# Kernel optimization log

Measured on AMD Instinct MI355X. Metric: run time of the kernel, lower is better.

Reference implementation:

```python
import jax, jax.numpy as jnp
import numpy as np
from jax.scipy.special import logsumexp

NUM_TAGS = 64
BATCH = 512
SEQ = 1024


def setup_inputs() -> dict:
    key = jax.random.key(0)
    k1, k2, k3, k4, k5 = jax.random.split(key, 5)
    emissions = jax.random.normal(k1, (BATCH, SEQ, NUM_TAGS), dtype=jnp.float32)
    # parameters: uniform(-0.1, 0.1) as in reset_parameters
    start_transitions = jax.random.uniform(k2, (NUM_TAGS,), minval=-0.1, maxval=0.1, dtype=jnp.float32)
    end_transitions = jax.random.uniform(k3, (NUM_TAGS,), minval=-0.1, maxval=0.1, dtype=jnp.float32)
    transitions = jax.random.uniform(k4, (NUM_TAGS, NUM_TAGS), minval=-0.1, maxval=0.1, dtype=jnp.float32)
    tags = jax.random.randint(k5, (BATCH, SEQ), 0, NUM_TAGS, dtype=jnp.int64)
    mask = jnp.ones((BATCH, SEQ), dtype=bool)
    return {"emissions": emissions, "start_transitions": start_transitions,
            "end_transitions": end_transitions, "transitions": transitions,
            "tags": tags, "mask": mask}


def _crf_loss(emissions, start_transitions, end_transitions, transitions, tags, mask):
    # batch_first=True -> move to time-major (S, B, T)
    emissions = jnp.transpose(emissions, (1, 0, 2))
    tags = tags.T
    mask = mask.T
    S, B, T = emissions.shape
    maskf = mask.astype(emissions.dtype)

    # ---- joint (numerator) score, fully vectorized ----
    em_sc = jnp.take_along_axis(emissions, tags[:, :, None], axis=2)[:, :, 0]  # [S, B]
    trans_sc = transitions[tags[:-1], tags[1:]]                                # [S-1, B]
    score = start_transitions[tags[0]] + em_sc[0]
    score = score + ((trans_sc + em_sc[1:]) * maskf[1:]).sum(axis=0)
    seq_ends = mask.astype(jnp.int32).sum(axis=0) - 1                          # [B]
    last_tags = tags[seq_ends, jnp.arange(B)]
    score = score + end_transitions[last_tags]

    # ---- log partition (denominator) via scan over time ----
    def step(alphas, xs):
        em_i, m_i = xs  # em_i: [B, T], m_i: [B]
        inner = alphas[:, :, None] + transitions[None, :, :] + em_i[:, None, :]  # [B, T, T]
        new_alphas = logsumexp(inner, axis=1)
        return jnp.where(m_i[:, None], new_alphas, alphas), None

    alphas0 = start_transitions + emissions[0]  # [B, T]
    alphas, _ = jax.lax.scan(step, alphas0, (emissions[1:], mask[1:]))
    log_z = logsumexp(alphas + end_transitions, axis=1)  # [B]

    return (log_z - score).sum()  # reduction='sum'


def reference(emissions, start_transitions, end_transitions, transitions, tags, mask):
    return _crf_loss(emissions, start_transitions, end_transitions, transitions, tags, mask)
```

## Files before the change

kernel.cpp:

```cpp
#include <hip/hip_runtime.h>

#define NT 64
#define SEQ 1024
#define BATCH 512

typedef _Float16 h2 __attribute__((ext_vector_type(2)));

__device__ __forceinline__ float rlf(float v, int lane) {
  return __int_as_float(__builtin_amdgcn_readlane(__float_as_int(v), lane));
}
__device__ __forceinline__ float bsum(float v) {
  #pragma unroll
  for (int m = 32; m; m >>= 1) v += __shfl_xor(v, m);
  return v;
}
__device__ __forceinline__ float dot2(h2 a, h2 b, float c) {
#if __has_builtin(__builtin_amdgcn_fdot2)
  return __builtin_amdgcn_fdot2(a, b, c, false);
#else
  return fmaf((float)a[0], (float)b[0], fmaf((float)a[1], (float)b[1], c));
#endif
}

template <int CTRL>
__device__ __forceinline__ unsigned dmov(unsigned v) {
  return (unsigned)__builtin_amdgcn_update_dpp(0, (int)v, CTRL, 0xF, 0xF, true);
}
#define DPP_SWAP1 0xB1
#define DPP_SWAP2 0x4E
#define DPP_ROR4  0x124
#define DPP_ROR8  0x128

__device__ __forceinline__ unsigned h2u(h2 v) { return __builtin_bit_cast(unsigned, v); }
__device__ __forceinline__ h2 u2h(unsigned v) { return __builtin_bit_cast(h2, v); }

#if __has_builtin(__builtin_amdgcn_permlane16_swap) && \
    __has_builtin(__builtin_amdgcn_permlane32_swap)
#define HAVE_PLSWAP 1
#else
#define HAVE_PLSWAP 0
#endif

__device__ __forceinline__ float xchg16(float x, bool use0) {
#if HAVE_PLSWAP
  const unsigned xb = __float_as_uint(x);
  auto r = __builtin_amdgcn_permlane16_swap(xb, xb, false, false);
  return __uint_as_float(use0 ? r[0] : r[1]);
#else
  return __shfl_xor(x, 16);
#endif
}
__device__ __forceinline__ float xchg32(float x, bool use0) {
#if HAVE_PLSWAP
  const unsigned xb = __float_as_uint(x);
  auto r = __builtin_amdgcn_permlane32_swap(xb, xb, false, false);
  return __uint_as_float(use0 ? r[0] : r[1]);
#else
  return __shfl_xor(x, 32);
#endif
}

__global__ __launch_bounds__(64) void crf_fwd(
    const float* __restrict__ em,
    const float* __restrict__ startT,
    const float* __restrict__ endT,
    const float* __restrict__ trans,
    const int*   __restrict__ tags,
    float* __restrict__ ws)
{
  const int b = blockIdx.x;
  const int j = threadIdx.x;

  __shared__ float sT[NT * NT];
  for (int i = j; i < NT * NT; i += NT) sT[i] = trans[i];
  __syncthreads();

  bool use0_16 = false, use0_32 = false;
#if HAVE_PLSWAP
  {
    const unsigned jb = (unsigned)j;
    auto a = __builtin_amdgcn_permlane16_swap(jb, jb, false, false);
    use0_16 = (a[0] == (jb ^ 16u));
    auto c = __builtin_amdgcn_permlane32_swap(jb, jb, false, false);
    use0_32 = (c[0] == (jb ^ 32u));
  }
#endif

  unsigned I[8];
  {
    unsigned tJ = dmov<DPP_SWAP1>((unsigned)j);
    I[0] = (unsigned)j | (tJ << 16);
    I[1] = dmov<DPP_SWAP2>(I[0]);
    I[2] = dmov<DPP_ROR4>(I[0]);
    I[3] = dmov<DPP_ROR4>(I[1]);
    I[4] = dmov<DPP_ROR8>(I[0]);
    I[5] = dmov<DPP_ROR8>(I[1]);
    I[6] = dmov<DPP_ROR8>(I[2]);
    I[7] = dmov<DPP_ROR8>(I[3]);
  }

  h2 eth[4][8];
  #pragma unroll
  for (int k = 0; k < 4; ++k) {
    const int col = j ^ (k << 4);
    #pragma unroll
    for (int r = 0; r < 8; ++r) {
      const int lo = (int)(I[r] & 0xFFFFu), hi = (int)(I[r] >> 16);
      h2 e;
      e[0] = (_Float16)(__expf(sT[lo * NT + col]) * 0.015625f);
      e[1] = (_Float16)(__expf(sT[hi * NT + col]) * 0.015625f);
      eth[k][r] = e;
    }
  }

  const float* emb = em + (size_t)b * SEQ * NT;
  const int*   tgb = tags + (size_t)b * SEQ;

  const float stv = startT[j];
  const float alpha0 = stv + emb[j];
  const float c0 = rlf(alpha0, 0);
  float nb = __expf(alpha0 - c0);

  float Crn = 0.0f;
  float rr = 1.0f;
  float lgrr = 0.0f;

  int tagv = tgb[j];
  const int tag0 = __builtin_amdgcn_readlane(tagv, 0);
  const float sc0 = rlf(stv, tag0);

  float scp = 0.0f;
  {
    int ptag = __shfl_up(tagv, 1);
    if (j > 0) scp += sT[ptag * NT + tagv];
    scp += emb[j * NT + tagv];
  }
  int carry = __builtin_amdgcn_readlane(tagv, 63);

  float embuf[8];
  #pragma unroll
  for (int k = 1; k <= 8; ++k) embuf[k & 7] = emb[k * NT + j];

  #define COLSUM(K, OUT) do {                       \
    float _a = dot2(g[0], eth[K][0], 0.0f);         \
    _a = dot2(g[1], eth[K][1], _a);                 \
    _a = dot2(g[2], eth[K][2], _a);                 \
    _a = dot2(g[3], eth[K][3], _a);                 \
    float _c = dot2(g[4], eth[K][4], 0.0f);         \
    _c = dot2(g[5], eth[K][5], _c);                 \
    _c = dot2(g[6], eth[K][6], _c);                 \
    _c = dot2(g[7], eth[K][7], _c);                 \
    OUT = _a + _c;                                  \
  } while (0)

  auto step = [&](int s, int slot) {
    const float em_cur = embuf[slot];
    int spre = s + 8;
    if (spre > SEQ - 1) spre = SEQ - 1;
    embuf[slot] = emb[(size_t)spre * NT + j];

    const float mm = __expf(em_cur - 0.5f) * rr;
    Crn -= lgrr;

    const float tv = __uint_as_float(dmov<DPP_SWAP1>(__float_as_uint(nb)));
    h2 pr;
    pr[0] = (_Float16)nb;
    pr[1] = (_Float16)tv;
    const unsigned G0 = h2u(pr);
    const unsigned G1 = dmov<DPP_SWAP2>(G0);
    const unsigned G2 = dmov<DPP_ROR4>(G0);
    const unsigned G3 = dmov<DPP_ROR4>(G1);
    const unsigned G4 = dmov<DPP_ROR8>(G0);
    const unsigned G5 = dmov<DPP_ROR8>(G1);
    const unsigned G6 = dmov<DPP_ROR8>(G2);
    const unsigned G7 = dmov<DPP_ROR8>(G3);
    const h2 g[8] = {u2h(G0), u2h(G1), u2h(G2), u2h(G3),
                     u2h(G4), u2h(G5), u2h(G6), u2h(G7)};

    float p0, p1, p2, p3;
    COLSUM(1, p1);
    COLSUM(3, p3);
    const float r1 = xchg16(p1, use0_16);
    const float r3 = xchg16(p3, use0_16);
    COLSUM(0, p0);
    COLSUM(2, p2);
    p0 += r1;
    p2 += r3;
    const float r2 = xchg32(p2, use0_32);
    p0 += r2;

    nb = p0 * mm;

    const float rv = rlf(nb, 0);
    rr = __builtin_amdgcn_rcpf(rv);
    lgrr = __logf(rr);
  };

  #pragma unroll 8
  for (int r = 1; r < NT; ++r) step(r, r & 7);

  for (int tb = 1; tb < SEQ / NT; ++tb) {
    tagv = tgb[tb * NT + j];
    int ptag = __shfl_up(tagv, 1);
    if (j == 0) ptag = carry;
    scp += sT[ptag * NT + tagv];
    const int base = tb * NT;
    scp += emb[(size_t)(base + j) * NT + tagv];
    carry = __builtin_amdgcn_readlane(tagv, 63);

    #pragma unroll 8
    for (int r = 0; r < NT; ++r) step(base + r, r & 7);
  }

  const float endv = endT[j];
  const float x = nb * __expf(endv);
  const float tot = bsum(x);
  const float Cbase = c0 + (float)(SEQ - 1) * (0.5f + 4.1588830833596715f);
  const float logz = Cbase + Crn + __logf(tot);

  const float sctot = bsum(scp);
  const float score = sc0 + sctot + rlf(endv, carry);

  if (j == 0) ws[b] = logz - score;
}

__global__ __launch_bounds__(64) void reduce_loss(const float* __restrict__ ws,
                                                  float* __restrict__ out) {
  const int t = threadIdx.x;
  float v = 0.f;
  #pragma unroll
  for (int k = 0; k < BATCH / 64; ++k) v += ws[k * 64 + t];
  const float tot = bsum(v);
  if (t == 0) out[0] = tot;
}

extern "C" void kernel_launch(void* const* d_in, const int* in_sizes, int n_in,
                              void* d_out, int out_size, void* d_ws, size_t ws_size,
                              hipStream_t stream) {
  const float* em    = (const float*)d_in[0];
  const float* st    = (const float*)d_in[1];
  const float* en    = (const float*)d_in[2];
  const float* tr    = (const float*)d_in[3];
  const int*   tags  = (const int*)d_in[4];

  float* ws  = (float*)d_ws;
  float* out = (float*)d_out;

  crf_fwd<<<BATCH, 64, 0, stream>>>(em, st, en, tr, tags, ws);
  reduce_loss<<<1, 64, 0, stream>>>(ws, out);
}
```

Before: 373.1 us.

## Process two batch sequences per wave with interleaved forward recurrences

Each 64-thread block now runs the forward-algorithm recurrence for two batch rows at once, interleaving their steps so the two independent dependency chains can hide each other's latency. The grid is halved to 256 blocks. The exp of the next emission is also computed one step early to take it off the critical path. In exchange, register pressure roughly doubles for the per-sequence state, and with only 256 waves on a 256-CU part each CU holds at most one wave.

```diff
diff --git a/kernel.cpp b/kernel.cpp
--- a/kernel.cpp
+++ b/kernel.cpp
@@ -60,7 +60,7 @@
 #endif
 }
 
-__global__ __launch_bounds__(64) void crf_fwd(
+__global__ __launch_bounds__(64, 1) void crf_fwd(
     const float* __restrict__ em,
     const float* __restrict__ startT,
     const float* __restrict__ endT,
@@ -68,7 +68,8 @@
     const int*   __restrict__ tags,
     float* __restrict__ ws)
 {
-  const int b = blockIdx.x;
+  const int bA = blockIdx.x;
+  const int bB = blockIdx.x + BATCH / 2;
   const int j = threadIdx.x;
 
   __shared__ float sT[NT * NT];
@@ -113,33 +114,53 @@
     }
   }
 
-  const float* emb = em + (size_t)b * SEQ * NT;
-  const int*   tgb = tags + (size_t)b * SEQ;
+  const float* embA = em + (size_t)bA * SEQ * NT;
+  const float* embB = em + (size_t)bB * SEQ * NT;
+  const int*   tgbA = tags + (size_t)bA * SEQ;
+  const int*   tgbB = tags + (size_t)bB * SEQ;
 
   const float stv = startT[j];
-  const float alpha0 = stv + emb[j];
-  const float c0 = rlf(alpha0, 0);
-  float nb = __expf(alpha0 - c0);
-
-  float Crn = 0.0f;
-  float rr = 1.0f;
-  float lgrr = 0.0f;
-
-  int tagv = tgb[j];
-  const int tag0 = __builtin_amdgcn_readlane(tagv, 0);
-  const float sc0 = rlf(stv, tag0);
-
-  float scp = 0.0f;
-  {
-    int ptag = __shfl_up(tagv, 1);
-    if (j > 0) scp += sT[ptag * NT + tagv];
-    scp += emb[j * NT + tagv];
-  }
-  int carry = __builtin_amdgcn_readlane(tagv, 63);
-
-  float embuf[8];
-  #pragma unroll
-  for (int k = 1; k <= 8; ++k) embuf[k & 7] = emb[k * NT + j];
+
+  const float alpha0A = stv + embA[j];
+  const float c0A = rlf(alpha0A, 0);
+  float nbA = __expf(alpha0A - c0A);
+  const float alpha0B = stv + embB[j];
+  const float c0B = rlf(alpha0B, 0);
+  float nbB = __expf(alpha0B - c0B);
+
+  float CrnA = 0.0f, rrA = 1.0f, lgrrA = 0.0f;
+  float CrnB = 0.0f, rrB = 1.0f, lgrrB = 0.0f;
+
+  int tagvA = tgbA[j];
+  const int tag0A = __builtin_amdgcn_readlane(tagvA, 0);
+  const float sc0A = rlf(stv, tag0A);
+  float scpA = 0.0f;
+  {
+    int ptag = __shfl_up(tagvA, 1);
+    if (j > 0) scpA += sT[ptag * NT + tagvA];
+    scpA += embA[j * NT + tagvA];
+  }
+  int carryA = __builtin_amdgcn_readlane(tagvA, 63);
+
+  int tagvB = tgbB[j];
+  const int tag0B = __builtin_amdgcn_readlane(tagvB, 0);
+  const float sc0B = rlf(stv, tag0B);
+  float scpB = 0.0f;
+  {
+    int ptag = __shfl_up(tagvB, 1);
+    if (j > 0) scpB += sT[ptag * NT + tagvB];
+    scpB += embB[j * NT + tagvB];
+  }
+  int carryB = __builtin_amdgcn_readlane(tagvB, 63);
+
+  float embufA[8], embufB[8];
+  #pragma unroll
+  for (int k = 1; k <= 8; ++k) embufA[k & 7] = embA[k * NT + j];
+  #pragma unroll
+  for (int k = 1; k <= 8; ++k) embufB[k & 7] = embB[k * NT + j];
+
+  float exqA = __expf(embufA[1] - 0.5f);
+  float exqB = __expf(embufB[1] - 0.5f);
 
   #define COLSUM(K, OUT) do {                       \
     float _a = dot2(g[0], eth[K][0], 0.0f);         \
@@ -153,75 +174,98 @@
     OUT = _a + _c;                                  \
   } while (0)
 
-  auto step = [&](int s, int slot) {
-    const float em_cur = embuf[slot];
-    int spre = s + 8;
-    if (spre > SEQ - 1) spre = SEQ - 1;
-    embuf[slot] = emb[(size_t)spre * NT + j];
-
-    const float mm = __expf(em_cur - 0.5f) * rr;
-    Crn -= lgrr;
-
-    const float tv = __uint_as_float(dmov<DPP_SWAP1>(__float_as_uint(nb)));
-    h2 pr;
-    pr[0] = (_Float16)nb;
-    pr[1] = (_Float16)tv;
-    const unsigned G0 = h2u(pr);
-    const unsigned G1 = dmov<DPP_SWAP2>(G0);
-    const unsigned G2 = dmov<DPP_ROR4>(G0);
-    const unsigned G3 = dmov<DPP_ROR4>(G1);
-    const unsigned G4 = dmov<DPP_ROR8>(G0);
-    const unsigned G5 = dmov<DPP_ROR8>(G1);
-    const unsigned G6 = dmov<DPP_ROR8>(G2);
-    const unsigned G7 = dmov<DPP_ROR8>(G3);
-    const h2 g[8] = {u2h(G0), u2h(G1), u2h(G2), u2h(G3),
-                     u2h(G4), u2h(G5), u2h(G6), u2h(G7)};
-
-    float p0, p1, p2, p3;
-    COLSUM(1, p1);
-    COLSUM(3, p3);
-    const float r1 = xchg16(p1, use0_16);
-    const float r3 = xchg16(p3, use0_16);
-    COLSUM(0, p0);
-    COLSUM(2, p2);
-    p0 += r1;
-    p2 += r3;
-    const float r2 = xchg32(p2, use0_32);
-    p0 += r2;
-
-    nb = p0 * mm;
-
-    const float rv = rlf(nb, 0);
-    rr = __builtin_amdgcn_rcpf(rv);
-    lgrr = __logf(rr);
-  };
+  #define STEP(S, s, slot) do {                                              \
+    const float ex_cur = exq##S;                                             \
+    int spre = (s) + 8;                                                      \
+    if (spre > SEQ - 1) spre = SEQ - 1;                                      \
+    const float em_next = embuf##S[((s) + 1) & 7];                           \
+    embuf##S[slot] = emb##S[(size_t)spre * NT + j];                          \
+    exq##S = __expf(em_next - 0.5f);                                         \
+    const float mm = ex_cur * rr##S;                                         \
+    Crn##S -= lgrr##S;                                                       \
+    const float tv =                                                         \
+        __uint_as_float(dmov<DPP_SWAP1>(__float_as_uint(nb##S)));            \
+    h2 pr;                                                                   \
+    pr[0] = (_Float16)nb##S;                                                 \
+    pr[1] = (_Float16)tv;                                                    \
+    const unsigned G0 = h2u(pr);                                             \
+    const unsigned G1 = dmov<DPP_SWAP2>(G0);                                 \
+    const unsigned G2 = dmov<DPP_ROR4>(G0);                                  \
+    const unsigned G3 = dmov<DPP_ROR4>(G1);                                  \
+    const unsigned G4 = dmov<DPP_ROR8>(G0);                                  \
+    const unsigned G5 = dmov<DPP_ROR8>(G1);                                  \
+    const unsigned G6 = dmov<DPP_ROR8>(G2);                                  \
+    const unsigned G7 = dmov<DPP_ROR8>(G3);                                  \
+    const h2 g[8] = {u2h(G0), u2h(G1), u2h(G2), u2h(G3),                     \
+                     u2h(G4), u2h(G5), u2h(G6), u2h(G7)};                    \
+    float p0, p1, p2, p3;                                                    \
+    COLSUM(1, p1);                                                           \
+    COLSUM(3, p3);                                                           \
+    const float r1 = xchg16(p1, use0_16);                                    \
+    const float r3 = xchg16(p3, use0_16);                                    \
+    COLSUM(0, p0);                                                           \
+    COLSUM(2, p2);                                                           \
+    p0 += r1;                                                                \
+    p2 += r3;                                                                \
+    const float r2 = xchg32(p2, use0_32);                                    \
+    p0 += r2;                                                                \
+    nb##S = p0 * mm;                                                         \
+    const float rv = rlf(nb##S, 0);                                          \
+    rr##S = __builtin_amdgcn_rcpf(rv);                                       \
+    lgrr##S = __logf(rr##S);                                                 \
+  } while (0)
 
   #pragma unroll 8
-  for (int r = 1; r < NT; ++r) step(r, r & 7);
+  for (int r = 1; r < NT; ++r) {
+    STEP(A, r, r & 7);
+    STEP(B, r, r & 7);
+  }
 
   for (int tb = 1; tb < SEQ / NT; ++tb) {
-    tagv = tgb[tb * NT + j];
-    int ptag = __shfl_up(tagv, 1);
-    if (j == 0) ptag = carry;
-    scp += sT[ptag * NT + tagv];
     const int base = tb * NT;
-    scp += emb[(size_t)(base + j) * NT + tagv];
-    carry = __builtin_amdgcn_readlane(tagv, 63);
+    tagvA = tgbA[base + j];
+    {
+      int ptag = __shfl_up(tagvA, 1);
+      if (j == 0) ptag = carryA;
+      scpA += sT[ptag * NT + tagvA];
+      scpA += embA[(size_t)(base + j) * NT + tagvA];
+    }
+    carryA = __builtin_amdgcn_readlane(tagvA, 63);
+
+    tagvB = tgbB[base + j];
+    {
+      int ptag = __shfl_up(tagvB, 1);
+      if (j == 0) ptag = carryB;
+      scpB += sT[ptag * NT + tagvB];
+      scpB += embB[(size_t)(base + j) * NT + tagvB];
+    }
+    carryB = __builtin_amdgcn_readlane(tagvB, 63);
 
     #pragma unroll 8
-    for (int r = 0; r < NT; ++r) step(base + r, r & 7);
+    for (int r = 0; r < NT; ++r) {
+      STEP(A, base + r, r & 7);
+      STEP(B, base + r, r & 7);
+    }
   }
 
   const float endv = endT[j];
-  const float x = nb * __expf(endv);
-  const float tot = bsum(x);
-  const float Cbase = c0 + (float)(SEQ - 1) * (0.5f + 4.1588830833596715f);
-  const float logz = Cbase + Crn + __logf(tot);
-
-  const float sctot = bsum(scp);
-  const float score = sc0 + sctot + rlf(endv, carry);
-
-  if (j == 0) ws[b] = logz - score;
+  const float Cbase = (float)(SEQ - 1) * (0.5f + 4.1588830833596715f);
+  {
+    const float x = nbA * __expf(endv);
+    const float tot = bsum(x);
+    const float logz = c0A + Cbase + CrnA + __logf(tot);
+    const float sctot = bsum(scpA);
+    const float score = sc0A + sctot + rlf(endv, carryA);
+    if (j == 0) ws[bA] = logz - score;
+  }
+  {
+    const float x = nbB * __expf(endv);
+    const float tot = bsum(x);
+    const float logz = c0B + Cbase + CrnB + __logf(tot);
+    const float sctot = bsum(scpB);
+    const float score = sc0B + sctot + rlf(endv, carryB);
+    if (j == 0) ws[bB] = logz - score;
+  }
 }
 
 __global__ __launch_bounds__(64) void reduce_loss(const float* __restrict__ ws,
@@ -246,6 +290,6 @@
   float* ws  = (float*)d_ws;
   float* out = (float*)d_out;
 
-  crf_fwd<<<BATCH, 64, 0, stream>>>(em, st, en, tr, tags, ws);
+  crf_fwd<<<BATCH / 2, 64, 0, stream>>>(em, st, en, tr, tags, ws);
   reduce_loss<<<1, 64, 0, stream>>>(ws, out);
 }
```

Measured after the change: 620.6 us. 66.3% more time.

## Double-buffer emission prefetch in 8-row groups and pipeline exp ahead of recurrence

Applied to the files above, without the earlier changes.

Replaces the per-step single-element prefetch ring with a double-buffered batch load of 8 emission rows per group, issued one group ahead. It also computes the exp of the next emission one step early so it sits off the serial dependency chain, and defers the gathered tag-emission and next-tag loads by a block to hide their latency. A launch_bounds occupancy hint of 1 is added. This should cut memory-latency stalls on the serial recurrence, at the cost of more registers.

```diff
diff --git a/kernel.cpp b/kernel.cpp
--- a/kernel.cpp
+++ b/kernel.cpp
@@ -60,7 +60,7 @@
 #endif
 }
 
-__global__ __launch_bounds__(64) void crf_fwd(
+__global__ __launch_bounds__(64, 1) void crf_fwd(
     const float* __restrict__ em,
     const float* __restrict__ startT,
     const float* __restrict__ endT,
@@ -128,89 +128,105 @@
   int tagv = tgb[j];
   const int tag0 = __builtin_amdgcn_readlane(tagv, 0);
   const float sc0 = rlf(stv, tag0);
-
   float scp = 0.0f;
   {
     int ptag = __shfl_up(tagv, 1);
     if (j > 0) scp += sT[ptag * NT + tagv];
-    scp += emb[j * NT + tagv];
   }
   int carry = __builtin_amdgcn_readlane(tagv, 63);
-
-  float embuf[8];
-  #pragma unroll
-  for (int k = 1; k <= 8; ++k) embuf[k & 7] = emb[k * NT + j];
-
-  #define COLSUM(K, OUT) do {                       \
-    float _a = dot2(g[0], eth[K][0], 0.0f);         \
-    _a = dot2(g[1], eth[K][1], _a);                 \
-    _a = dot2(g[2], eth[K][2], _a);                 \
-    _a = dot2(g[3], eth[K][3], _a);                 \
-    float _c = dot2(g[4], eth[K][4], 0.0f);         \
-    _c = dot2(g[5], eth[K][5], _c);                 \
-    _c = dot2(g[6], eth[K][6], _c);                 \
-    _c = dot2(g[7], eth[K][7], _c);                 \
-    OUT = _a + _c;                                  \
+  float gpend = emb[(size_t)j * NT + tagv];
+  int tagv_nxt = tgb[NT + j];
+
+  float bufA[8], bufB[8];
+  #pragma unroll
+  for (int k = 0; k < 8; ++k) bufA[k] = emb[k * NT + j];
+
+  float exq = __expf(bufA[1] - 0.5f);
+
+  #define COLSUM(K, OUT) do {                         \
+    float _a = dot2(u2h(G0), eth[K][0], 0.0f);        \
+    _a = dot2(u2h(G1), eth[K][1], _a);                \
+    _a = dot2(u2h(G2), eth[K][2], _a);                \
+    _a = dot2(u2h(G3), eth[K][3], _a);                \
+    float _c = dot2(u2h(G4), eth[K][4], 0.0f);        \
+    _c = dot2(u2h(G5), eth[K][5], _c);                \
+    _c = dot2(u2h(G6), eth[K][6], _c);                \
+    _c = dot2(u2h(G7), eth[K][7], _c);                \
+    OUT = _a + _c;                                    \
   } while (0)
 
-  auto step = [&](int s, int slot) {
-    const float em_cur = embuf[slot];
-    int spre = s + 8;
-    if (spre > SEQ - 1) spre = SEQ - 1;
-    embuf[slot] = emb[(size_t)spre * NT + j];
-
-    const float mm = __expf(em_cur - 0.5f) * rr;
-    Crn -= lgrr;
-
-    const float tv = __uint_as_float(dmov<DPP_SWAP1>(__float_as_uint(nb)));
-    h2 pr;
-    pr[0] = (_Float16)nb;
-    pr[1] = (_Float16)tv;
-    const unsigned G0 = h2u(pr);
-    const unsigned G1 = dmov<DPP_SWAP2>(G0);
-    const unsigned G2 = dmov<DPP_ROR4>(G0);
-    const unsigned G3 = dmov<DPP_ROR4>(G1);
-    const unsigned G4 = dmov<DPP_ROR8>(G0);
-    const unsigned G5 = dmov<DPP_ROR8>(G1);
-    const unsigned G6 = dmov<DPP_ROR8>(G2);
-    const unsigned G7 = dmov<DPP_ROR8>(G3);
-    const h2 g[8] = {u2h(G0), u2h(G1), u2h(G2), u2h(G3),
-                     u2h(G4), u2h(G5), u2h(G6), u2h(G7)};
-
-    float p0, p1, p2, p3;
-    COLSUM(1, p1);
-    COLSUM(3, p3);
-    const float r1 = xchg16(p1, use0_16);
-    const float r3 = xchg16(p3, use0_16);
-    COLSUM(0, p0);
-    COLSUM(2, p2);
-    p0 += r1;
-    p2 += r3;
-    const float r2 = xchg32(p2, use0_32);
-    p0 += r2;
-
-    nb = p0 * mm;
-
-    const float rv = rlf(nb, 0);
-    rr = __builtin_amdgcn_rcpf(rv);
-    lgrr = __logf(rr);
-  };
-
-  #pragma unroll 8
-  for (int r = 1; r < NT; ++r) step(r, r & 7);
+  #define STEP(EMN) do {                                                     \
+    const float ex_cur = exq;                                                \
+    exq = __expf((EMN)-0.5f);                                                \
+    const float mm = ex_cur * rr;                                            \
+    Crn -= lgrr;                                                             \
+    const float tv =                                                         \
+        __uint_as_float(dmov<DPP_SWAP1>(__float_as_uint(nb)));               \
+    h2 pr;                                                                   \
+    pr[0] = (_Float16)nb;                                                    \
+    pr[1] = (_Float16)tv;                                                    \
+    const unsigned G0 = h2u(pr);                                             \
+    const unsigned G1 = dmov<DPP_SWAP2>(G0);                                 \
+    const unsigned G2 = dmov<DPP_ROR4>(G0);                                  \
+    const unsigned G3 = dmov<DPP_ROR4>(G1);                                  \
+    const unsigned G4 = dmov<DPP_ROR8>(G0);                                  \
+    const unsigned G5 = dmov<DPP_ROR8>(G1);                                  \
+    const unsigned G6 = dmov<DPP_ROR8>(G2);                                  \
+    const unsigned G7 = dmov<DPP_ROR8>(G3);                                  \
+    float p0, p1, p2, p3;                                                    \
+    COLSUM(1, p1);                                                           \
+    COLSUM(3, p3);                                                           \
+    const float r1 = xchg16(p1, use0_16);                                    \
+    const float r3 = xchg16(p3, use0_16);                                    \
+    COLSUM(0, p0);                                                           \
+    COLSUM(2, p2);                                                           \
+    p0 += r1;                                                                \
+    p2 += r3;                                                                \
+    const float r2 = xchg32(p2, use0_32);                                    \
+    p0 += r2;                                                                \
+    nb = p0 * mm;                                                            \
+    const float rv = rlf(nb, 0);                                             \
+    rr = __builtin_amdgcn_rcpf(rv);                                          \
+    lgrr = __logf(rr);                                                       \
+  } while (0)
+
+  #define GROUP(CUR, NXT, GIDX, FIRSTK) do {                                 \
+    int prow_ = ((GIDX) + 1) * 8;                                            \
+    if (prow_ > SEQ - 8) prow_ = SEQ - 8;        \
+    const float* pf_ = emb + (size_t)prow_ * NT;                             \
+    _Pragma("unroll")                                                        \
+    for (int k_ = 0; k_ < 8; ++k_) NXT[k_] = pf_[k_ * NT + j];               \
+    _Pragma("unroll")                                                        \
+    for (int k_ = FIRSTK; k_ < 8; ++k_) {                                    \
+      const float emn_ = (k_ < 7) ? CUR[k_ + 1] : NXT[0];                    \
+      STEP(emn_);                                                            \
+    }                                                                        \
+  } while (0)
+
+  GROUP(bufA, bufB, 0, 1);
+  GROUP(bufB, bufA, 1, 0);
+  for (int pr2 = 1; pr2 < 4; ++pr2) {
+    GROUP(bufA, bufB, 2 * pr2 + 0, 0);
+    GROUP(bufB, bufA, 2 * pr2 + 1, 0);
+  }
 
   for (int tb = 1; tb < SEQ / NT; ++tb) {
-    tagv = tgb[tb * NT + j];
-    int ptag = __shfl_up(tagv, 1);
+    scp += gpend;
+    const int tagv_new = tagv_nxt;
+    if (tb < SEQ / NT - 1) tagv_nxt = tgb[(tb + 1) * NT + j];
+    int ptag = __shfl_up(tagv_new, 1);
     if (j == 0) ptag = carry;
-    scp += sT[ptag * NT + tagv];
-    const int base = tb * NT;
-    scp += emb[(size_t)(base + j) * NT + tagv];
-    carry = __builtin_amdgcn_readlane(tagv, 63);
-
-    #pragma unroll 8
-    for (int r = 0; r < NT; ++r) step(base + r, r & 7);
-  }
+    scp += sT[ptag * NT + tagv_new];
+    carry = __builtin_amdgcn_readlane(tagv_new, 63);
+    gpend = emb[(size_t)(tb * NT + j) * NT + tagv_new];
+
+    const int g0 = tb * 8;
+    for (int pr2 = 0; pr2 < 4; ++pr2) {
+      GROUP(bufA, bufB, g0 + 2 * pr2 + 0, 0);
+      GROUP(bufB, bufA, g0 + 2 * pr2 + 1, 0);
+    }
+  }
+  scp += gpend;
 
   const float endv = endT[j];
   const float x = nb * __expf(endv);
```

Measured after the change: 367.3 us. About the same (-1.5%).
